# Kernel tuning notes

Hardware: AMD Instinct MI355X
Metric: run time of the kernel (lower is better)

## Reference

```python
import jax, jax.numpy as jnp
import numpy as np

N, D = 8192, 768
EPS = 1e-5  # torch LayerNorm default


def setup_inputs() -> dict:
    key = jax.random.key(0)
    ks = jax.random.split(key, 5)
    q = jax.random.normal(ks[0], (N, D), dtype=jnp.float32)
    k = jax.random.normal(ks[1], (N, D), dtype=jnp.float32)
    v = jax.random.normal(ks[2], (N, D), dtype=jnp.float32)
    ln_w = jnp.ones((D,), dtype=jnp.float32)
    ln_b = jnp.zeros((D,), dtype=jnp.float32)
    W_qkv = jax.random.normal(ks[3], (D, D), dtype=jnp.float32) * 0.02
    W_proj = jax.random.normal(ks[4], (D, D), dtype=jnp.float32) * 0.02
    b_proj = jnp.zeros((D,), dtype=jnp.float32)
    return {"q": q, "k": k, "v": v, "ln_w": ln_w, "ln_b": ln_b,
            "W_qkv": W_qkv, "W_proj": W_proj, "b_proj": b_proj}


def reference(q, k, v, ln_w, ln_b, W_qkv, W_proj, b_proj):
    dim = q.shape[-1]
    scale = dim ** (-0.5)

    def ln(x):
        mu = jnp.mean(x, axis=-1, keepdims=True)
        var = jnp.mean((x - mu) ** 2, axis=-1, keepdims=True)
        return (x - mu) * jax.lax.rsqrt(var + EPS) * ln_w + ln_b

    # shared LayerNorm + shared Linear (toto0, no bias) applied to q, k, v
    qn = ln(q) @ W_qkv.T  # [N, D]
    kn = ln(k) @ W_qkv.T
    vn = ln(v) @ W_qkv.T

    attn = jnp.einsum('qc,kc->qk', qn, kn) * scale  # [N, N]
    attn = jax.nn.softmax(attn, axis=-1)
    out = jnp.einsum('qk,kc->qc', attn, vn)  # [N, D]
    out = out @ W_proj.T + b_proj  # proj0
    return out
```

## Files before the change

### kernel.cpp

```cpp
#include <hip/hip_runtime.h>
#include <hip/hip_bf16.h>
#include <stdint.h>

typedef short bf16x8 __attribute__((ext_vector_type(8)));
typedef float f32x4 __attribute__((ext_vector_type(4)));
typedef unsigned short u16;
typedef u16 u16x8 __attribute__((ext_vector_type(8)));

__device__ __forceinline__ u16 f2bf(float x) {
  __hip_bfloat16 h = __float2bfloat16(x);
  return *reinterpret_cast<u16*>(&h);
}
__device__ __forceinline__ float bf2f(u16 v) {
  unsigned u = (unsigned)v << 16;
  return *reinterpret_cast<float*>(&u);
}

__device__ __forceinline__ void gload_lds16(const void* g, const void* lds_base) {
  __builtin_amdgcn_global_load_lds(
      (const __attribute__((address_space(1))) unsigned int*)(uintptr_t)g,
      (__attribute__((address_space(3))) unsigned int*)(uintptr_t)lds_base,
      16, 0, 0);
}

#define BAR() __builtin_amdgcn_s_barrier()
#define LG0() asm volatile("s_waitcnt lgkmcnt(0)" ::: "memory")
#define VM0() asm volatile("s_waitcnt vmcnt(0)" ::: "memory")

__global__ __launch_bounds__(256) void ln_cast_kernel(
    const float* __restrict__ q, const float* __restrict__ k, const float* __restrict__ v,
    const float* __restrict__ lw, const float* __restrict__ lb, u16* __restrict__ out) {
  int row = blockIdx.x;
  const float* x;
  if (row < 8192) x = q + (size_t)row * 768;
  else if (row < 16384) x = k + (size_t)(row - 8192) * 768;
  else x = v + (size_t)(row - 16384) * 768;
  int t = threadIdx.x;
  float a0 = x[t], a1 = x[t + 256], a2 = x[t + 512];
  __shared__ float red[4];
  __shared__ float red2[4];
  float s = a0 + a1 + a2;
  for (int o = 32; o; o >>= 1) s += __shfl_down(s, o, 64);
  if ((t & 63) == 0) red[t >> 6] = s;
  __syncthreads();
  float mean = (red[0] + red[1] + red[2] + red[3]) * (1.0f / 768.0f);
  float d0 = a0 - mean, d1 = a1 - mean, d2 = a2 - mean;
  float vs = d0 * d0 + d1 * d1 + d2 * d2;
  for (int o = 32; o; o >>= 1) vs += __shfl_down(vs, o, 64);
  if ((t & 63) == 0) red2[t >> 6] = vs;
  __syncthreads();
  float var = (red2[0] + red2[1] + red2[2] + red2[3]) * (1.0f / 768.0f);
  float rstd = rsqrtf(var + 1e-5f);
  u16* o_ = out + (size_t)row * 768;
  o_[t]       = f2bf(d0 * rstd * lw[t]       + lb[t]);
  o_[t + 256] = f2bf(d1 * rstd * lw[t + 256] + lb[t + 256]);
  o_[t + 512] = f2bf(d2 * rstd * lw[t + 512] + lb[t + 512]);
}

__global__ __launch_bounds__(256) void cast_f32_bf16(const float* __restrict__ in,
                                                     u16* __restrict__ out, int n4) {
  int i = blockIdx.x * 256 + threadIdx.x;
  if (i < n4) {
    float4 vv = ((const float4*)in)[i];
    ushort4 o;
    o.x = f2bf(vv.x); o.y = f2bf(vv.y); o.z = f2bf(vv.z); o.w = f2bf(vv.w);
    ((ushort4*)out)[i] = o;
  }
}

__global__ __launch_bounds__(256) void zero_f32(float* __restrict__ p, int n) {
  int i = blockIdx.x * 256 + threadIdx.x;
  if (i < n) p[i] = 0.0f;
}

__global__ __launch_bounds__(256) void transpose64(const u16* __restrict__ in, u16* __restrict__ out) {
  __shared__ __align__(16) u16 tile[64][72];
  int b = blockIdx.x;
  int tr = b / 12, tc = b % 12;
  int t = threadIdx.x;
  int r = t >> 3;
  int cb = (t & 7) << 3;
#pragma unroll
  for (int i = 0; i < 2; i++) {
    int row = r + i * 32;
    const u16* src = in + (size_t)(tr * 64 + row) * 768 + tc * 64 + cb;
    *(uint4*)&tile[row][cb] = *(const uint4*)src;
  }
  __syncthreads();
#pragma unroll
  for (int i = 0; i < 2; i++) {
    int oc = r + i * 32;
    u16x8 tmp;
#pragma unroll
    for (int j = 0; j < 8; j++) tmp[j] = tile[cb + j][oc];
    u16* dst = out + (size_t)(tc * 64 + oc) * 8192 + tr * 64 + cb;
    *(u16x8*)dst = tmp;
  }
}

__global__ __launch_bounds__(256) void reduce4_scale(
    const u16* __restrict__ p0, const u16* __restrict__ p1,
    const u16* __restrict__ p2, const u16* __restrict__ p3,
    const float* __restrict__ rowsum, u16* __restrict__ out, int n8) {
  int i = blockIdx.x * 256 + threadIdx.x;
  if (i < n8) {
    float inv = 1.0f / rowsum[i / 96];
    u16x8 a = ((const u16x8*)p0)[i];
    u16x8 b = ((const u16x8*)p1)[i];
    u16x8 c = ((const u16x8*)p2)[i];
    u16x8 d = ((const u16x8*)p3)[i];
    u16x8 o;
#pragma unroll
    for (int j = 0; j < 8; j++)
      o[j] = f2bf((bf2f(a[j]) + bf2f(b[j]) + bf2f(c[j]) + bf2f(d[j])) * inv);
    ((u16x8*)out)[i] = o;
  }
}

__global__ __launch_bounds__(512, 2) void qk_exp_256(
    const u16* __restrict__ A, const u16* __restrict__ B, u16* __restrict__ C,
    float* __restrict__ rowsum, float scale) {
  __shared__ __align__(16) u16 sA[2][256 * 64];
  __shared__ __align__(16) u16 sB[2][256 * 64];
  int orig = blockIdx.x;
  int wg = (orig & 7) * 128 + (orig >> 3);
  int tm = wg >> 5, tn = wg & 31;
  const int t = threadIdx.x, l = t & 63, w = t >> 6;
  const int wr = w >> 2, wc = w & 3;
  const int lr = l & 15, lq = l >> 4;
  const int colb = lq * 16;
  const int rswz = (lr & 7) << 4;

  f32x4 acc[8][4];
#pragma unroll
  for (int m = 0; m < 8; m++)
#pragma unroll
    for (int n = 0; n < 4; n++) acc[m][n] = (f32x4){0.f, 0.f, 0.f, 0.f};

  const size_t rA0 = (size_t)tm * 256, rB0 = (size_t)tn * 256;

  auto SCALL = [&](int bufsel, int T, int idx) {
    const u16* src = (idx < 4) ? A : B;
    size_t r0 = (idx < 4) ? rA0 : rB0;
    u16* dstbase = (idx < 4) ? sA[bufsel] : sB[bufsel];
    int p = idx & 3, k0 = T << 6;
    int x = p * 8192 + t * 16;
    int r = x >> 7;
    int cb = (x & 127) ^ ((r & 7) << 4);
    gload_lds16((const char*)(src + (r0 + r) * 768 + k0) + cb,
                (const char*)dstbase + p * 8192 + w * 1024);
  };
  auto LOADA = [&](bf16x8 (&aF)[4], int d, int mh, int kk) {
#pragma unroll
    for (int mf = 0; mf < 4; mf++) {
      int arow = wr * 128 + (mh * 4 + mf) * 16 + lr;
      int x = arow * 128 + kk * 64 + colb;
      aF[mf] = *(const bf16x8*)((const char*)sA[d] + (x ^ rswz));
    }
  };
  auto LOADB = [&](bf16x8 (&bF)[4], int d, int kk) {
#pragma unroll
    for (int nf = 0; nf < 4; nf++) {
      int brow = wc * 64 + nf * 16 + lr;
      int x = brow * 128 + kk * 64 + colb;
      bF[nf] = *(const bf16x8*)((const char*)sB[d] + (x ^ rswz));
    }
  };
  auto MM = [&](bf16x8 (&aF)[4], bf16x8 (&bF)[4], int mh) {
    __builtin_amdgcn_s_setprio(1);
#pragma unroll
    for (int mf = 0; mf < 4; mf++)
#pragma unroll
      for (int nf = 0; nf < 4; nf++)
        acc[mh * 4 + mf][nf] = __builtin_amdgcn_mfma_f32_16x16x32_bf16(
            aF[mf], bF[nf], acc[mh * 4 + mf][nf], 0, 0, 0);
    __builtin_amdgcn_s_setprio(0);
  };

#pragma unroll
  for (int idx = 0; idx < 8; idx++) SCALL(0, 0, idx);
  VM0();
  BAR();

  for (int T = 0; T < 12; T++) {
    const int cur = T & 1, nxt = cur ^ 1;
    const bool pf = (T < 11);
    bf16x8 aF[4], bF0[4], bF1[4];
    LOADA(aF, cur, 0, 0); LOADB(bF0, cur, 0);
    if (pf) { SCALL(nxt, T + 1, 0); SCALL(nxt, T + 1, 1); }
    BAR(); LG0(); MM(aF, bF0, 0); BAR();
    LOADA(aF, cur, 1, 0);
    if (pf) { SCALL(nxt, T + 1, 2); SCALL(nxt, T + 1, 3); }
    BAR(); LG0(); MM(aF, bF0, 1); BAR();
    LOADA(aF, cur, 0, 1); LOADB(bF1, cur, 1);
    if (pf) { SCALL(nxt, T + 1, 4); SCALL(nxt, T + 1, 5); }
    BAR(); LG0(); MM(aF, bF1, 0); BAR();
    LOADA(aF, cur, 1, 1);
    if (pf) { SCALL(nxt, T + 1, 6); SCALL(nxt, T + 1, 7); }
    BAR(); LG0(); MM(aF, bF1, 1);
    VM0();
    BAR();
  }

  float rs[8][4];
#pragma unroll
  for (int m = 0; m < 8; m++)
#pragma unroll
    for (int j = 0; j < 4; j++) rs[m][j] = 0.0f;
  const size_t rowBase = rA0 + (size_t)wr * 128;
  const int colBase = tn * 256 + wc * 64;
#pragma unroll
  for (int mi = 0; mi < 8; mi++) {
    size_t row0 = rowBase + mi * 16 + lq * 4;
#pragma unroll
    for (int nf = 0; nf < 4; nf++) {
      int col = colBase + nf * 16 + lr;
#pragma unroll
      for (int j = 0; j < 4; j++) {
        float e = __expf(acc[mi][nf][j] * scale);
        C[(row0 + j) * 8192 + col] = f2bf(e);
        rs[mi][j] += e;
      }
    }
  }
#pragma unroll
  for (int mi = 0; mi < 8; mi++)
#pragma unroll
    for (int j = 0; j < 4; j++) {
      float r = rs[mi][j];
      r += __shfl_xor(r, 1); r += __shfl_xor(r, 2);
      r += __shfl_xor(r, 4); r += __shfl_xor(r, 8);
      if (lr == 0) atomicAdd(&rowsum[rowBase + mi * 16 + lq * 4 + j], r);
    }
}

template <int MODE>
__global__ __launch_bounds__(256, 2) void gemm_bt(
    const u16* __restrict__ A0, const u16* __restrict__ B0,
    void* __restrict__ Cv0, void* __restrict__ Cv1,
    int M, int N, int K, int lda, int ldb, int ldc,
    float scale, const float* __restrict__ bias, size_t cSplitStride) {
  __shared__ __align__(16) u16 sA[128 * 64];
  __shared__ __align__(16) u16 sB[128 * 64];
  const int z = blockIdx.y;
  const u16* A = A0 + (size_t)z * (size_t)K;
  const u16* B = B0 + (size_t)z * (size_t)K;
  u16* Cb = (z < 2) ? ((u16*)Cv0 + (size_t)z * cSplitStride)
                    : ((u16*)Cv1 + (size_t)(z - 2) * cSplitStride);
  const int nTn = N >> 7;
  int nwg = gridDim.x, orig = blockIdx.x;
  int qq = nwg >> 3, rr = nwg & 7;
  int xcd = orig & 7, loc = orig >> 3;
  int wg = (xcd < rr ? xcd * (qq + 1) : rr * (qq + 1) + (xcd - rr) * qq) + loc;
  int tm = wg / nTn, tn = wg % nTn;

  const int t = threadIdx.x, l = t & 63, w = t >> 6;
  const int wr = w >> 1, wc = w & 1;
  const int lr = l & 15, kg = (l >> 4) << 3;

  f32x4 acc[4][4];
#pragma unroll
  for (int m = 0; m < 4; m++)
#pragma unroll
    for (int n = 0; n < 4; n++) acc[m][n] = (f32x4){0.f, 0.f, 0.f, 0.f};

  const size_t rowA0 = (size_t)tm * 128;
  const size_t rowB0 = (size_t)tn * 128;
  const int nk = K >> 6;
  for (int kt = 0; kt < nk; kt++) {
    const int k0 = kt << 6;
#pragma unroll
    for (int i = 0; i < 4; i++) {
      int chunk = i * 256 + t;
      int row = chunk >> 3;
      int col = (chunk & 7) << 3;
      gload_lds16(A + (rowA0 + row) * lda + k0 + col, (const char*)sA + (i * 256 + w * 64) * 16);
      gload_lds16(B + (rowB0 + row) * ldb + k0 + col, (const char*)sB + (i * 256 + w * 64) * 16);
    }
    __syncthreads();
#pragma unroll
    for (int kk = 0; kk < 2; kk++) {
      bf16x8 af[4], bfv[4];
#pragma unroll
      for (int m = 0; m < 4; m++)
        af[m] = *(const bf16x8*)&sA[(wr * 64 + m * 16 + lr) * 64 + kk * 32 + kg];
#pragma unroll
      for (int n = 0; n < 4; n++)
        bfv[n] = *(const bf16x8*)&sB[(wc * 64 + n * 16 + lr) * 64 + kk * 32 + kg];
#pragma unroll
      for (int m = 0; m < 4; m++)
#pragma unroll
        for (int n = 0; n < 4; n++)
          acc[m][n] = __builtin_amdgcn_mfma_f32_16x16x32_bf16(af[m], bfv[n], acc[m][n], 0, 0, 0);
    }
    __syncthreads();
  }
#pragma unroll
  for (int m = 0; m < 4; m++) {
    int row = tm * 128 + wr * 64 + m * 16 + ((l >> 4) << 2);
#pragma unroll
    for (int n = 0; n < 4; n++) {
      int col = tn * 128 + wc * 64 + n * 16 + lr;
#pragma unroll
      for (int j = 0; j < 4; j++) {
        float vl = acc[m][n][j];
        if (MODE == 0) Cb[(size_t)(row + j) * ldc + col] = f2bf(vl * scale);
        else ((float*)Cv0)[(size_t)(row + j) * ldc + col] = vl + bias[col];
      }
    }
  }
}

extern "C" void kernel_launch(void* const* d_in, const int* in_sizes, int n_in,
                              void* d_out, int out_size, void* d_ws, size_t ws_size,
                              hipStream_t stream) {
  const float* q  = (const float*)d_in[0];
  const float* k  = (const float*)d_in[1];
  const float* v  = (const float*)d_in[2];
  const float* lw = (const float*)d_in[3];
  const float* lb = (const float*)d_in[4];
  const float* Wq = (const float*)d_in[5];
  const float* Wp = (const float*)d_in[6];
  const float* bp = (const float*)d_in[7];

  char* ws = (char*)d_ws;
  size_t off = 0;
  auto alloc = [&](size_t b) { size_t o = off; off += (b + 255) & ~(size_t)255; return o; };
  size_t o_ln = alloc((size_t)24576 * 768 * 2);
  size_t o_pj = alloc((size_t)24576 * 768 * 2);
  size_t o_wq = alloc((size_t)768 * 768 * 2);
  size_t o_wp = alloc((size_t)768 * 768 * 2);
  u16* lnbuf = (u16*)(ws + o_ln);
  u16* pj    = (u16*)(ws + o_pj);
  u16* wqb   = (u16*)(ws + o_wq);
  u16* wpb   = (u16*)(ws + o_wp);
  const size_t NS = (size_t)8192 * 768;
  u16* vnT = lnbuf;
  u16* p0  = lnbuf + NS;
  u16* p1  = lnbuf + 2 * NS;
  float* rowsum = (float*)(pj + 2 * NS);
  u16* p2 = (u16*)d_out;
  u16* p3 = p2 + NS;
  size_t fixedEnd = off;
  u16* Sbuf = (u16*)(ws + fixedEnd);

  const float scale = 0.03608439182435161f;

  ln_cast_kernel<<<dim3(24576), dim3(256), 0, stream>>>(q, k, v, lw, lb, lnbuf);
  cast_f32_bf16<<<dim3(576), dim3(256), 0, stream>>>(Wq, wqb, 147456);
  cast_f32_bf16<<<dim3(576), dim3(256), 0, stream>>>(Wp, wpb, 147456);

  gemm_bt<0><<<dim3(1152), dim3(256), 0, stream>>>(lnbuf, wqb, (void*)pj, (void*)pj,
      24576, 768, 768, 768, 768, 768, 1.0f, (const float*)nullptr, 0);

  transpose64<<<dim3(1536), dim3(256), 0, stream>>>(pj + (size_t)16384 * 768, vnT);
  zero_f32<<<dim3(32), dim3(256), 0, stream>>>(rowsum, 8192);

  qk_exp_256<<<dim3(1024), dim3(512), 0, stream>>>(pj, pj + NS, Sbuf, rowsum, scale);

  gemm_bt<0><<<dim3(384, 4), dim3(256), 0, stream>>>(
      Sbuf, vnT, (void*)p0, (void*)p2,
      8192, 768, 2048, 8192, 8192, 768, 1.0f, (const float*)nullptr, NS);

  reduce4_scale<<<dim3(3072), dim3(256), 0, stream>>>(p0, p1, p2, p3, rowsum, p0, (int)(NS / 8));

  gemm_bt<2><<<dim3(384), dim3(256), 0, stream>>>(p0, wpb, d_out, d_out,
      8192, 768, 768, 768, 768, 768, 1.0f, bp, 0);
}
```

Before: 398.4 us.

## Use 4-stage K=32 LDS ring with prefetch distance 2 in QK GEMM

Reworks the QK^T GEMM main loop to stage 32-wide K slices in a 4-buffer LDS ring, issuing global-to-LDS loads two iterations ahead and waiting with vmcnt(4) instead of draining all loads each step. Barriers per K step drop from four to two and a new XOR swizzle suits the 64-byte rows. The block-to-tile mapping also changes so that each XCD handles 4 contiguous row tiles, aiming for better L2 reuse. The trade-off is twice as many loop iterations and reliance on the compiler not inserting its own full waits around the LDS reads.

```diff
diff --git a/kernel.cpp b/kernel.cpp
--- a/kernel.cpp
+++ b/kernel.cpp
@@ -24,8 +24,6 @@
 }
 
 #define BAR() __builtin_amdgcn_s_barrier()
-#define LG0() asm volatile("s_waitcnt lgkmcnt(0)" ::: "memory")
-#define VM0() asm volatile("s_waitcnt vmcnt(0)" ::: "memory")
 
 __global__ __launch_bounds__(256) void ln_cast_kernel(
     const float* __restrict__ q, const float* __restrict__ k, const float* __restrict__ v,
@@ -120,16 +118,15 @@
 __global__ __launch_bounds__(512, 2) void qk_exp_256(
     const u16* __restrict__ A, const u16* __restrict__ B, u16* __restrict__ C,
     float* __restrict__ rowsum, float scale) {
-  __shared__ __align__(16) u16 sA[2][256 * 64];
-  __shared__ __align__(16) u16 sB[2][256 * 64];
+  __shared__ __align__(16) u16 sA[4][256 * 32];
+  __shared__ __align__(16) u16 sB[4][256 * 32];
   int orig = blockIdx.x;
-  int wg = (orig & 7) * 128 + (orig >> 3);
-  int tm = wg >> 5, tn = wg & 31;
+  int xcd = orig & 7, i = orig >> 3;
+  int tm = xcd * 4 + (i & 3), tn = i >> 2;
   const int t = threadIdx.x, l = t & 63, w = t >> 6;
   const int wr = w >> 2, wc = w & 3;
   const int lr = l & 15, lq = l >> 4;
   const int colb = lq * 16;
-  const int rswz = (lr & 7) << 4;
 
   f32x4 acc[8][4];
 #pragma unroll
@@ -139,31 +136,31 @@
 
   const size_t rA0 = (size_t)tm * 256, rB0 = (size_t)tn * 256;
 
-  auto SCALL = [&](int bufsel, int T, int idx) {
-    const u16* src = (idx < 4) ? A : B;
-    size_t r0 = (idx < 4) ? rA0 : rB0;
-    u16* dstbase = (idx < 4) ? sA[bufsel] : sB[bufsel];
-    int p = idx & 3, k0 = T << 6;
+  auto SCALL = [&](int b, int Tn, int idx) {
+    const u16* src = (idx < 2) ? A : B;
+    size_t r0 = (idx < 2) ? rA0 : rB0;
+    char* dst = (char*)((idx < 2) ? sA[b] : sB[b]);
+    int p = idx & 1;
     int x = p * 8192 + t * 16;
-    int r = x >> 7;
-    int cb = (x & 127) ^ ((r & 7) << 4);
-    gload_lds16((const char*)(src + (r0 + r) * 768 + k0) + cb,
-                (const char*)dstbase + p * 8192 + w * 1024);
+    int r = x >> 6;
+    int cb = (x & 63) ^ (((r >> 1) & 3) << 4);
+    gload_lds16((const char*)(src + (r0 + r) * 768 + (Tn << 5)) + cb,
+                dst + p * 8192 + w * 1024);
   };
-  auto LOADA = [&](bf16x8 (&aF)[4], int d, int mh, int kk) {
+  auto LOADA = [&](bf16x8 (&aF)[4], int d, int mh) {
 #pragma unroll
     for (int mf = 0; mf < 4; mf++) {
-      int arow = wr * 128 + (mh * 4 + mf) * 16 + lr;
-      int x = arow * 128 + kk * 64 + colb;
-      aF[mf] = *(const bf16x8*)((const char*)sA[d] + (x ^ rswz));
+      int row = wr * 128 + (mh * 4 + mf) * 16 + lr;
+      int x = row * 64 + colb;
+      aF[mf] = *(const bf16x8*)((const char*)sA[d] + (x ^ (((row >> 1) & 3) << 4)));
     }
   };
-  auto LOADB = [&](bf16x8 (&bF)[4], int d, int kk) {
+  auto LOADB = [&](bf16x8 (&bF)[4], int d) {
 #pragma unroll
     for (int nf = 0; nf < 4; nf++) {
-      int brow = wc * 64 + nf * 16 + lr;
-      int x = brow * 128 + kk * 64 + colb;
-      bF[nf] = *(const bf16x8*)((const char*)sB[d] + (x ^ rswz));
+      int row = wc * 64 + nf * 16 + lr;
+      int x = row * 64 + colb;
+      bF[nf] = *(const bf16x8*)((const char*)sB[d] + (x ^ (((row >> 1) & 3) << 4)));
     }
   };
   auto MM = [&](bf16x8 (&aF)[4], bf16x8 (&bF)[4], int mh) {
@@ -178,27 +175,30 @@
   };
 
 #pragma unroll
-  for (int idx = 0; idx < 8; idx++) SCALL(0, 0, idx);
-  VM0();
+  for (int idx = 0; idx < 4; idx++) SCALL(0, 0, idx);
+#pragma unroll
+  for (int idx = 0; idx < 4; idx++) SCALL(1, 1, idx);
+  asm volatile("s_waitcnt vmcnt(4)" ::: "memory");
   BAR();
 
-  for (int T = 0; T < 12; T++) {
-    const int cur = T & 1, nxt = cur ^ 1;
-    const bool pf = (T < 11);
-    bf16x8 aF[4], bF0[4], bF1[4];
-    LOADA(aF, cur, 0, 0); LOADB(bF0, cur, 0);
-    if (pf) { SCALL(nxt, T + 1, 0); SCALL(nxt, T + 1, 1); }
-    BAR(); LG0(); MM(aF, bF0, 0); BAR();
-    LOADA(aF, cur, 1, 0);
-    if (pf) { SCALL(nxt, T + 1, 2); SCALL(nxt, T + 1, 3); }
-    BAR(); LG0(); MM(aF, bF0, 1); BAR();
-    LOADA(aF, cur, 0, 1); LOADB(bF1, cur, 1);
-    if (pf) { SCALL(nxt, T + 1, 4); SCALL(nxt, T + 1, 5); }
-    BAR(); LG0(); MM(aF, bF1, 0); BAR();
-    LOADA(aF, cur, 1, 1);
-    if (pf) { SCALL(nxt, T + 1, 6); SCALL(nxt, T + 1, 7); }
-    BAR(); LG0(); MM(aF, bF1, 1);
-    VM0();
+#pragma unroll 4
+  for (int T = 0; T < 24; T++) {
+    const int cur = T & 3;
+    bf16x8 aF[4], bF[4];
+    LOADA(aF, cur, 0);
+    LOADB(bF, cur);
+    if (T + 2 < 24) {
+      const int nb = (T + 2) & 3;
+      SCALL(nb, T + 2, 0); SCALL(nb, T + 2, 1);
+      SCALL(nb, T + 2, 2); SCALL(nb, T + 2, 3);
+    }
+    BAR();
+    MM(aF, bF, 0);
+    bf16x8 aG[4];
+    LOADA(aG, cur, 1);
+    MM(aG, bF, 1);
+    if (T < 22) { asm volatile("s_waitcnt vmcnt(4)" ::: "memory"); }
+    else        { asm volatile("s_waitcnt vmcnt(0)" ::: "memory"); }
     BAR();
   }
 
```

Result: faster. 362.5 us (-9.0%).
